# Kernel optimization log

Measured on AMD Instinct MI355X. Metric: run time of the kernel, lower is better.

The kernel has to match this reference:

```python
import jax, jax.numpy as jnp
import numpy as np

N, IC, IH, IW = 8, 128, 32, 32
OC, H, KH, KW = 32, 256, 2, 2


def setup_inputs() -> dict:
    key = jax.random.key(0)
    ks = jax.random.split(key, 7)
    s1 = 1.0 / np.sqrt(IC)
    s2 = 1.0 / np.sqrt(H)
    x = jax.random.normal(ks[0], (N, IC, IH, IW), dtype=jnp.float32)
    # per-output-channel MLP params, stacked along oC (torch Linear-style uniform init)
    W1 = jax.random.uniform(ks[1], (OC, IC, H), jnp.float32, -s1, s1)
    b1 = jax.random.uniform(ks[2], (OC, H), jnp.float32, -s1, s1)
    W2 = jax.random.uniform(ks[3], (OC, H, H), jnp.float32, -s2, s2)
    b2 = jax.random.uniform(ks[4], (OC, H), jnp.float32, -s2, s2)
    W3 = jax.random.uniform(ks[5], (OC, H, KH * KW), jnp.float32, -s2, s2)
    b3 = jax.random.uniform(ks[6], (OC, KH * KW), jnp.float32, -s2, s2)
    return {"x": x, "W1": W1, "b1": b1, "W2": W2, "b2": b2, "W3": W3, "b3": b3}


def reference(x, W1, b1, W2, b2, W3, b3):
    n, iC, iH, iW = x.shape
    oC = W1.shape[0]
    kH, kW = KH, KW
    # per-pixel features: [n, iH, iW, iC]
    pix = jnp.transpose(x, (0, 2, 3, 1))
    # batched 3-layer MLP over stacked oC channels (single grouped GEMM per layer)
    h1 = jax.nn.relu(jnp.einsum('nijc,ocd->onijd', pix, W1) + b1[:, None, None, None, :])
    h2 = jax.nn.relu(jnp.einsum('onijd,ode->onije', h1, W2) + b2[:, None, None, None, :])
    out = jnp.einsum('onije,oek->onijk', h2, W3) + b3[:, None, None, None, :]
    # [oC, n, iH, iW, kH, kW] -> [n, oC, iH, kH, iW, kW] -> [n, oC, oH, oW]
    out = out.reshape(oC, n, iH, iW, kH, kW)
    out = jnp.transpose(out, (1, 0, 2, 4, 3, 5)).reshape(n, oC, kH * iH, kW * iW)
    return out
```

## Files before the change

kernel.cpp:

```cpp
#include <hip/hip_runtime.h>
#include <hip/hip_bf16.h>


#define IC    128
#define IHW   1024
#define OCH   32
#define HDIM  256

typedef float  f32x4  __attribute__((ext_vector_type(4)));
typedef float  f32x2  __attribute__((ext_vector_type(2)));
typedef __bf16 bf16x8 __attribute__((ext_vector_type(8)));
typedef unsigned short us8 __attribute__((ext_vector_type(8)));
typedef unsigned int u32;

static __device__ __forceinline__ unsigned short f2bf(float f) {
  __hip_bfloat16 h = __float2bfloat16(f);
  return __builtin_bit_cast(unsigned short, h);
}

static __device__ __forceinline__ u32 cvtpk(float lo, float hi) {
  u32 r;
  asm("v_cvt_pk_bf16_f32 %0, %1, %2" : "=v"(r) : "v"(lo), "v"(hi));
  return r;
}

static __device__ __forceinline__ bf16x8 ld16(const unsigned short* p) {
  return __builtin_bit_cast(bf16x8, *reinterpret_cast<const uint4*>(p));
}

static __device__ __forceinline__ void gl_lds16(const unsigned short* g, char* l) {
  __builtin_amdgcn_global_load_lds(
      (const __attribute__((address_space(1))) u32*)g,
      (__attribute__((address_space(3))) u32*)l,
      16, 0, 0);
}

static __device__ void transpose_dev(const float* __restrict__ src,
                                     unsigned short* __restrict__ dst,
                                     int NR, int NC, int nrt, int nct,
                                     int bid, int t, float* tl)
{
  const int ct = bid % nct;
  const int rt = (bid / nct) % nrt;
  const int b  = bid / (nct * nrt);

  const float* sb = src + ((size_t)b * NR + (rt << 6)) * NC + (ct << 6);
  const int col = (t & 15) << 2;
  const int rq  = t >> 4;
#pragma unroll
  for (int rr = 0; rr < 4; ++rr) {
    int row = (rr << 4) + rq;
    f32x4 v = *reinterpret_cast<const f32x4*>(sb + row * NC + col);
#pragma unroll
    for (int i = 0; i < 4; ++i) tl[row * 65 + col + i] = v[i];
  }
  __syncthreads();

  unsigned short* db = dst + ((size_t)b * NC + (ct << 6)) * NR + (rt << 6);
  const int r0 = (t & 7) << 3;
  const int cq = t >> 3;
#pragma unroll
  for (int cr = 0; cr < 2; ++cr) {
    int c = (cr << 5) + cq;
    us8 vv;
#pragma unroll
    for (int i = 0; i < 8; ++i) vv[i] = f2bf(tl[(r0 + i) * 65 + c]);
    *reinterpret_cast<us8*>(db + (size_t)c * NR + r0) = vv;
  }
}

__global__ __launch_bounds__(256) void prepass_k(
    const float* __restrict__ x,  unsigned short* __restrict__ pix,
    const float* __restrict__ W1, unsigned short* __restrict__ W1t,
    const float* __restrict__ W2, unsigned short* __restrict__ W2t,
    const float* __restrict__ W3, unsigned short* __restrict__ W3t)
{
  __shared__ float tl[64 * 65];
  const int bid = blockIdx.x;
  const int t   = threadIdx.x;
  if (bid < 256) {
    transpose_dev(x, pix, 128, 1024, 2, 16, bid, t, tl);
  } else if (bid < 512) {
    transpose_dev(W1, W1t, 128, 256, 2, 4, bid - 256, t, tl);
  } else if (bid < 1024) {
    transpose_dev(W2, W2t, 256, 256, 4, 4, bid - 512, t, tl);
  } else {
    int idx = ((bid - 1024) << 8) + t;
    int k = idx & 255, nn = (idx >> 8) & 15, o = idx >> 12;
    W3t[idx] = (nn < 4) ? f2bf(W3[(o * HDIM + k) * 4 + nn]) : (unsigned short)0;
  }
}


#define LDB(dst, buf, ROW, ks)                                                   \
  _Pragma("unroll")                                                              \
  for (int mf = 0; mf < 2; ++mf) {                                               \
    int m = (mf << 4) + l15;                                                     \
    dst[mf] = *reinterpret_cast<const bf16x8*>(                                  \
        (buf) + ((((m << (ROW)) + ((ks) << 6) + (kgrp << 1))) ^ ((l15 & 7) << 4)));\
  }

#define MF4(WR, KS, BP)                                                          \
  __builtin_amdgcn_s_setprio(1);                                                 \
  _Pragma("unroll")                                                              \
  for (int nf = 0; nf < 2; ++nf)                                                 \
    _Pragma("unroll")                                                            \
    for (int mf = 0; mf < 2; ++mf)                                               \
      acc[nf][mf] = __builtin_amdgcn_mfma_f32_16x16x32_bf16(WR[nf][KS], BP[mf], acc[nf][mf], 0, 0, 0); \
  __builtin_amdgcn_s_setprio(0);

#define EPI(dst)                                                                 \
  _Pragma("unroll")                                                              \
  for (int nf = 0; nf < 2; ++nf) {                                               \
    int n0 = wnb + (nf << 4) + (lg << 2);                                        \
    _Pragma("unroll")                                                            \
    for (int mf = 0; mf < 2; ++mf) {                                             \
      int m = (mf << 4) + l15;                                                   \
      uint2 hv;                                                                  \
      hv.x = cvtpk(fmaxf(acc[nf][mf][0], 0.f), fmaxf(acc[nf][mf][1], 0.f));      \
      hv.y = cvtpk(fmaxf(acc[nf][mf][2], 0.f), fmaxf(acc[nf][mf][3], 0.f));      \
      *reinterpret_cast<uint2*>(                                                 \
          (dst) + (((m << 9) + (n0 << 1)) ^ ((l15 & 7) << 4))) = hv;             \
    }                                                                            \
  }

#define INIT_ACC(BB)                                                             \
  _Pragma("unroll")                                                              \
  for (int nf = 0; nf < 2; ++nf)                                                 \
    _Pragma("unroll")                                                            \
    for (int mf = 0; mf < 2; ++mf) acc[nf][mf] = BB[nf];

#define STAGE(PXB, BUF)                                                          \
  {                                                                              \
    int m = t >> 4, c16 = t & 15;                                                \
    gl_lds16(pix + (size_t)((PXB) + m) * IC + ((c16 ^ (m & 7)) << 3),            \
             (BUF) + t * 16);                                                    \
  }

#define PIPE_BARRIER(N)                                                          \
  asm volatile("s_waitcnt vmcnt(" #N ") lgkmcnt(0)" ::: "memory");               \
  __builtin_amdgcn_sched_barrier(0);                                             \
  __builtin_amdgcn_s_barrier();                                                  \
  __builtin_amdgcn_sched_barrier(0);

__global__ __launch_bounds__(512, 2) void fused_mlp_k(
    const unsigned short* __restrict__ pix,
    const unsigned short* __restrict__ W1t,
    const unsigned short* __restrict__ W2t,
    const unsigned short* __restrict__ W3t,
    const float* __restrict__ b1,
    const float* __restrict__ b2,
    const float* __restrict__ b3f,
    float* __restrict__ out)
{
  __shared__ __align__(16) char lds[90112];
  const int t    = threadIdx.x;
  const int lane = t & 63;
  const int w    = t >> 6;
  const int bx   = blockIdx.x;
  const int o    = ((bx & 7) << 2) | ((bx >> 3) & 3);
  const int pixbase = (bx >> 5) << 8;

  const int l15  = lane & 15;
  const int lg   = lane >> 4;
  const int kgrp = lg << 3;
  const int wnb  = w << 5;

  char* pixb[3] = { lds, lds + 8192, lds + 16384 };
  char* h1b[2]  = { lds + 24576, lds + 40960 };
  char* h2b[2]  = { lds + 57344, lds + 73728 };

  STAGE(pixbase,      pixb[0])
  STAGE(pixbase + 32, pixb[1])
  STAGE(pixbase + 64, pixb[2])

  const unsigned short* W1p = W1t + (o << 15) + (wnb + l15) * IC + kgrp;
  const unsigned short* W2p = W2t + (o << 16) + (wnb + l15) * HDIM + kgrp;
  bf16x8 W1r[2][4], W2r[2][8], W3r[8];
#pragma unroll
  for (int nf = 0; nf < 2; ++nf)
#pragma unroll
    for (int ks = 0; ks < 4; ++ks)
      W1r[nf][ks] = ld16(W1p + (nf << 4) * IC + (ks << 5));
#pragma unroll
  for (int nf = 0; nf < 2; ++nf)
#pragma unroll
    for (int ks = 0; ks < 8; ++ks)
      W2r[nf][ks] = ld16(W2p + (nf << 4) * HDIM + (ks << 5));
#pragma unroll
  for (int ks = 0; ks < 8; ++ks)
    W3r[ks] = ld16(W3t + (o << 12) + l15 * HDIM + (ks << 5) + kgrp);

  f32x4 bb1[2], bb2[2];
#pragma unroll
  for (int nf = 0; nf < 2; ++nf) {
    bb1[nf] = *reinterpret_cast<const f32x4*>(b1 + (o << 8) + wnb + (nf << 4) + (lg << 2));
    bb2[nf] = *reinterpret_cast<const f32x4*>(b2 + (o << 8) + wnb + (nf << 4) + (lg << 2));
  }
  const f32x4 b3v = *reinterpret_cast<const f32x4*>(b3f + (o << 2));
  const f32x4 vzero = {0.f, 0.f, 0.f, 0.f};

  f32x4 acc[2][2];
  bf16x8 bp[2], bq[2];

  __syncthreads();

  INIT_ACC(bb1)
  LDB(bp, pixb[0], 8, 0)
  LDB(bq, pixb[0], 8, 1) MF4(W1r, 0, bp)
  LDB(bp, pixb[0], 8, 2) MF4(W1r, 1, bq)
  LDB(bq, pixb[0], 8, 3) MF4(W1r, 2, bp)
                         MF4(W1r, 3, bq)
  EPI(h1b[0])
  __syncthreads();

#pragma unroll
  for (int i = 0; i <= 8; ++i) {
    if (i <= 7) {
      char* src = h1b[i & 1];
      INIT_ACC(bb2)
      LDB(bp, src, 9, 0)
      LDB(bq, src, 9, 1) MF4(W2r, 0, bp)
      LDB(bp, src, 9, 2) MF4(W2r, 1, bq)
      LDB(bq, src, 9, 3) MF4(W2r, 2, bp)
      LDB(bp, src, 9, 4) MF4(W2r, 3, bq)
      LDB(bq, src, 9, 5) MF4(W2r, 4, bp)
      LDB(bp, src, 9, 6) MF4(W2r, 5, bq)
      LDB(bq, src, 9, 7) MF4(W2r, 6, bp)
                         MF4(W2r, 7, bq)
      EPI(h2b[i & 1])
    }

    if (i >= 1 && w < 2) {
      const char* hs = h2b[(i - 1) & 1];
      const int m3 = (w << 4) + l15;
      f32x4 a3a = b3v;
      f32x4 a3b = {0.f, 0.f, 0.f, 0.f};
#pragma unroll
      for (int ks = 0; ks < 8; ks += 2) {
        bf16x8 bh0 = *reinterpret_cast<const bf16x8*>(
            hs + (((m3 << 9) + (ks << 6) + (kgrp << 1)) ^ ((l15 & 7) << 4)));
        bf16x8 bh1 = *reinterpret_cast<const bf16x8*>(
            hs + (((m3 << 9) + ((ks + 1) << 6) + (kgrp << 1)) ^ ((l15 & 7) << 4)));
        a3a = __builtin_amdgcn_mfma_f32_16x16x32_bf16(W3r[ks],     bh0, a3a, 0, 0, 0);
        a3b = __builtin_amdgcn_mfma_f32_16x16x32_bf16(W3r[ks + 1], bh1, a3b, 0, 0, 0);
      }
      if (lane < 16) {
        int pixel = pixbase + ((i - 1) << 5) + m3;
        int n = pixel >> 10, p = pixel & 1023;
        int ii = p >> 5, jj = p & 31;
        float* ob = out + ((size_t)((n << 5) + o) << 12) + (ii << 7) + (jj << 1);
        f32x2 r0 = { a3a[0] + a3b[0], a3a[1] + a3b[1] };
        f32x2 r1 = { a3a[2] + a3b[2], a3a[3] + a3b[3] };
        *reinterpret_cast<f32x2*>(ob) = r0;
        *reinterpret_cast<f32x2*>(ob + 64) = r1;
      }
    }

    if (i <= 4) STAGE(pixbase + ((i + 3) << 5), pixb[i % 3])

    if (i <= 6) {
      char* psrc = pixb[(i + 1) % 3];
      INIT_ACC(bb1)
      LDB(bp, psrc, 8, 0)
      LDB(bq, psrc, 8, 1) MF4(W1r, 0, bp)
      LDB(bp, psrc, 8, 2) MF4(W1r, 1, bq)
      LDB(bq, psrc, 8, 3) MF4(W1r, 2, bp)
                          MF4(W1r, 3, bq)
      EPI(h1b[(i + 1) & 1])
    }

    if (i <= 4) { PIPE_BARRIER(1) } else { PIPE_BARRIER(0) }
  }
}

extern "C" void kernel_launch(void* const* d_in, const int* in_sizes, int n_in,
                              void* d_out, int out_size, void* d_ws, size_t ws_size,
                              hipStream_t stream) {
  const float* x  = (const float*)d_in[0];
  const float* W1 = (const float*)d_in[1];
  const float* b1 = (const float*)d_in[2];
  const float* W2 = (const float*)d_in[3];
  const float* b2 = (const float*)d_in[4];
  const float* W3 = (const float*)d_in[5];
  const float* b3 = (const float*)d_in[6];
  float* out = (float*)d_out;

  char* ws = (char*)d_ws;
  unsigned short* pixw = (unsigned short*)(ws);
  unsigned short* W1t  = (unsigned short*)(ws + (size_t)(2u << 20));
  unsigned short* W2t  = (unsigned short*)(ws + (size_t)(4u << 20));
  unsigned short* W3t  = (unsigned short*)(ws + (size_t)(8u << 20));

  prepass_k<<<1536, 256, 0, stream>>>(x, pixw, W1, W1t, W2, W2t, W3, W3t);
  fused_mlp_k<<<1024, 512, 0, stream>>>(pixw, W1t, W2t, W3t, b1, b2, b3, out);
}
```

Baseline: 86.13 us.

## Shrink LDS buffers and restructure pipeline to raise blocks per CU

Reduces shared memory from three pixel buffers and double-buffered h1 to two pixel buffers and a single h1 buffer. The loop schedule is reordered, with an extra barrier per iteration so the single h1 buffer is safe, and launch bounds request four blocks per CU. The aim is higher occupancy to hide latency. In exchange it adds synchronization, loses some overlap, and the tighter register budget may force spilling of the register-resident weights.

```diff
diff --git a/kernel.cpp b/kernel.cpp
--- a/kernel.cpp
+++ b/kernel.cpp
@@ -143,7 +143,7 @@
   __builtin_amdgcn_s_barrier();                                                  \
   __builtin_amdgcn_sched_barrier(0);
 
-__global__ __launch_bounds__(512, 2) void fused_mlp_k(
+__global__ __launch_bounds__(512, 4) void fused_mlp_k(
     const unsigned short* __restrict__ pix,
     const unsigned short* __restrict__ W1t,
     const unsigned short* __restrict__ W2t,
@@ -153,7 +153,7 @@
     const float* __restrict__ b3f,
     float* __restrict__ out)
 {
-  __shared__ __align__(16) char lds[90112];
+  __shared__ __align__(16) char lds[65536];
   const int t    = threadIdx.x;
   const int lane = t & 63;
   const int w    = t >> 6;
@@ -166,13 +166,12 @@
   const int kgrp = lg << 3;
   const int wnb  = w << 5;
 
-  char* pixb[3] = { lds, lds + 8192, lds + 16384 };
-  char* h1b[2]  = { lds + 24576, lds + 40960 };
-  char* h2b[2]  = { lds + 57344, lds + 73728 };
+  char* pixb[2] = { lds, lds + 8192 };
+  char* h1      = lds + 16384;
+  char* h2b[2]  = { lds + 32768, lds + 49152 };
 
   STAGE(pixbase,      pixb[0])
   STAGE(pixbase + 32, pixb[1])
-  STAGE(pixbase + 64, pixb[2])
 
   const unsigned short* W1p = W1t + (o << 15) + (wnb + l15) * IC + kgrp;
   const unsigned short* W2p = W2t + (o << 16) + (wnb + l15) * HDIM + kgrp;
@@ -198,7 +197,6 @@
     bb2[nf] = *reinterpret_cast<const f32x4*>(b2 + (o << 8) + wnb + (nf << 4) + (lg << 2));
   }
   const f32x4 b3v = *reinterpret_cast<const f32x4*>(b3f + (o << 2));
-  const f32x4 vzero = {0.f, 0.f, 0.f, 0.f};
 
   f32x4 acc[2][2];
   bf16x8 bp[2], bq[2];
@@ -211,24 +209,37 @@
   LDB(bp, pixb[0], 8, 2) MF4(W1r, 1, bq)
   LDB(bq, pixb[0], 8, 3) MF4(W1r, 2, bp)
                          MF4(W1r, 3, bq)
-  EPI(h1b[0])
+  EPI(h1)
   __syncthreads();
 
 #pragma unroll
   for (int i = 0; i <= 8; ++i) {
     if (i <= 7) {
-      char* src = h1b[i & 1];
       INIT_ACC(bb2)
-      LDB(bp, src, 9, 0)
-      LDB(bq, src, 9, 1) MF4(W2r, 0, bp)
-      LDB(bp, src, 9, 2) MF4(W2r, 1, bq)
-      LDB(bq, src, 9, 3) MF4(W2r, 2, bp)
-      LDB(bp, src, 9, 4) MF4(W2r, 3, bq)
-      LDB(bq, src, 9, 5) MF4(W2r, 4, bp)
-      LDB(bp, src, 9, 6) MF4(W2r, 5, bq)
-      LDB(bq, src, 9, 7) MF4(W2r, 6, bp)
-                         MF4(W2r, 7, bq)
+      LDB(bp, h1, 9, 0)
+      LDB(bq, h1, 9, 1) MF4(W2r, 0, bp)
+      LDB(bp, h1, 9, 2) MF4(W2r, 1, bq)
+      LDB(bq, h1, 9, 3) MF4(W2r, 2, bp)
+      LDB(bp, h1, 9, 4) MF4(W2r, 3, bq)
+      LDB(bq, h1, 9, 5) MF4(W2r, 4, bp)
+      LDB(bp, h1, 9, 6) MF4(W2r, 5, bq)
+      LDB(bq, h1, 9, 7) MF4(W2r, 6, bp)
+                        MF4(W2r, 7, bq)
       EPI(h2b[i & 1])
+    }
+    if (i <= 5) STAGE(pixbase + ((i + 2) << 5), pixb[i & 1])
+
+    if (i <= 5) { PIPE_BARRIER(1) } else { PIPE_BARRIER(0) }
+
+    if (i <= 6) {
+      char* psrc = pixb[(i + 1) & 1];
+      INIT_ACC(bb1)
+      LDB(bp, psrc, 8, 0)
+      LDB(bq, psrc, 8, 1) MF4(W1r, 0, bp)
+      LDB(bp, psrc, 8, 2) MF4(W1r, 1, bq)
+      LDB(bq, psrc, 8, 3) MF4(W1r, 2, bp)
+                          MF4(W1r, 3, bq)
+      EPI(h1)
     }
 
     if (i >= 1 && w < 2) {
@@ -257,20 +268,9 @@
       }
     }
 
-    if (i <= 4) STAGE(pixbase + ((i + 3) << 5), pixb[i % 3])
-
-    if (i <= 6) {
-      char* psrc = pixb[(i + 1) % 3];
-      INIT_ACC(bb1)
-      LDB(bp, psrc, 8, 0)
-      LDB(bq, psrc, 8, 1) MF4(W1r, 0, bp)
-      LDB(bp, psrc, 8, 2) MF4(W1r, 1, bq)
-      LDB(bq, psrc, 8, 3) MF4(W1r, 2, bp)
-                          MF4(W1r, 3, bq)
-      EPI(h1b[(i + 1) & 1])
-    }
-
-    if (i <= 4) { PIPE_BARRIER(1) } else { PIPE_BARRIER(0) }
+    if (i < 8) {
+      if (i <= 5) { PIPE_BARRIER(1) } else { PIPE_BARRIER(0) }
+    }
   }
 }
 
```

After: 289.5 us. +236.1%, slower.
